# Performance work log

Hardware: AMD Instinct MI355X
Metric: run time of the kernel (lower is better)

## Reference

```python
import jax, jax.numpy as jnp
import numpy as np

NUM_BINS = 15
THRESHOLD = 0.01


def setup_inputs() -> dict:
    key = jax.random.key(0)
    k1, k2 = jax.random.split(key)
    N, C = 500000, 100
    probas = jax.random.uniform(k1, (N, C), dtype=jnp.float32)
    labels = jax.random.randint(k2, (N,), 0, C, dtype=jnp.int64)
    return {"probas": probas, "labels": labels}


def reference(probas, labels):
    # probas: [N, C] float, labels: [N] int
    N, C = probas.shape
    B = NUM_BINS
    bins = jnp.linspace(0.0, 1.0, B + 1, dtype=probas.dtype)  # [B+1]

    # bin index: bins[lo] <= p < bins[lo+1] (side='right' => right edge strict)
    lo = jnp.searchsorted(bins, probas, side='right') - 1      # [N, C]
    lo_c = jnp.clip(lo, 0, B - 1)
    left_edge = bins[lo_c]
    # original uses strict inequalities on BOTH edges, plus threshold filter
    valid = (probas > THRESHOLD) & (lo >= 0) & (lo < B) & (probas > left_edge)
    w = valid.astype(probas.dtype)                              # [N, C]

    # segment id = class * B + bin, flattened over [N, C]
    cols = jnp.broadcast_to(jnp.arange(C), (N, C))
    seg = (cols * B + lo_c).ravel()
    num_seg = C * B

    correct = (labels[:, None] == jnp.arange(C)[None, :]).astype(probas.dtype)

    count = jax.ops.segment_sum(w.ravel(), seg, num_segments=num_seg)
    sum_p = jax.ops.segment_sum((probas * w).ravel(), seg, num_segments=num_seg)
    sum_a = jax.ops.segment_sum((correct * w).ravel(), seg, num_segments=num_seg)

    nan = jnp.asarray(jnp.nan, probas.dtype)
    denom = jnp.maximum(count, 1.0)
    confs = jnp.where(count > 0, sum_p / denom, nan).reshape(C, B)
    accs = jnp.where(count > 0, sum_a / denom, nan).reshape(C, B)
    n_samples = count.reshape(C, B)
    return confs, accs, n_samples
```

## Files before the change

kernel.cpp:

```cpp
#include <hip/hip_runtime.h>

#define NBINS 15
#define NCLS  100
#define NSEG  (NBINS * NCLS)
#define NGRP  64
#define MAXBLK 2048
#define BLK   256
#define SUMSCALE 2048.0f
#define INV15 (1.0f / 15.0f)

typedef float nf4 __attribute__((ext_vector_type(4)));

__device__ __forceinline__ void proc_f4(nf4 v, int i,
                                        const int* __restrict__ labels,
                                        unsigned int* s_pk, unsigned int* s_ac)
{
    int row  = i / 25;
    int col0 = (i - row * 25) * 4;
    int lbl  = labels[row];
    float pv[4] = {v.x, v.y, v.z, v.w};
    #pragma unroll
    for (int j = 0; j < 4; ++j) {
        float p = pv[j];
        int c = col0 + j;
        int k = (int)(p * 15.0f);
        if (k < NBINS && (float)(k + 1) * INV15 <= p)      ++k;
        else if (k > 0 && (float)k * INV15 > p)            --k;
        float left = (float)k * INV15;
        if (p > 0.01f && k < NBINS && p > left) {
            int seg = c * NBINS + k;
            unsigned int pk = (1u << 20) | (unsigned int)(p * SUMSCALE + 0.5f);
            atomicAdd(&s_pk[seg], pk);
            if (lbl == c) atomicAdd(&s_ac[seg], 1u);
        }
    }
}

__global__ __launch_bounds__(BLK) void calib_accum(
    const float* __restrict__ probas,
    const int*   __restrict__ labels,
    unsigned int* __restrict__ partU,
    int total4)
{
    __shared__ unsigned int s_pk[NSEG];
    __shared__ unsigned int s_ac[NSEG];
    const int t = threadIdx.x;
    for (int i = t; i < NSEG; i += BLK) { s_pk[i] = 0u; s_ac[i] = 0u; }
    __syncthreads();

    const nf4* __restrict__ p4 = (const nf4*)probas;
    const int stride = gridDim.x * BLK;
    const int half4  = total4 >> 1;

    for (int i = blockIdx.x * BLK + t; i < half4; i += stride) {
        nf4 a = __builtin_nontemporal_load(&p4[i]);
        nf4 b = __builtin_nontemporal_load(&p4[i + half4]);
        proc_f4(a, i,         labels, s_pk, s_ac);
        proc_f4(b, i + half4, labels, s_pk, s_ac);
    }
    if ((total4 & 1) && blockIdx.x == 0 && t == 0) {
        proc_f4(p4[total4 - 1], total4 - 1, labels, s_pk, s_ac);
    }
    __syncthreads();

    unsigned int* dst = partU + (size_t)blockIdx.x * (2 * NSEG);
    for (int s = t; s < NSEG; s += BLK) {
        dst[s]        = s_pk[s];
        dst[NSEG + s] = s_ac[s];
    }
}

__global__ __launch_bounds__(256) void calib_mid(
    const unsigned int* __restrict__ partU, int nblk, int chunk,
    unsigned int*       __restrict__ partB)
{
    int t = blockIdx.x * 256 + threadIdx.x;
    if (t >= NGRP * NSEG) return;
    int g = t / NSEG;
    int s = t - g * NSEG;
    int b0 = g * chunk;
    int b1 = b0 + chunk; if (b1 > nblk) b1 = nblk;
    unsigned int cnt = 0u, sumq = 0u, acc = 0u;
    for (int b = b0; b < b1; ++b) {
        const unsigned int* src = partU + (size_t)b * (2 * NSEG);
        unsigned int pk = src[s];
        cnt  += pk >> 20;
        sumq += pk & 0xFFFFFu;
        acc  += src[NSEG + s];
    }
    unsigned int* dst = partB + (size_t)g * (3 * NSEG);
    dst[s]            = cnt;
    dst[NSEG + s]     = sumq;
    dst[2 * NSEG + s] = acc;
}

__global__ __launch_bounds__(256) void calib_fin(
    const unsigned int* __restrict__ partB,
    float*              __restrict__ out)
{
    int s = blockIdx.x * 256 + threadIdx.x;
    if (s >= NSEG) return;
    unsigned int cnt = 0u, sumq = 0u, acc = 0u;
    #pragma unroll
    for (int g = 0; g < NGRP; ++g) {
        const unsigned int* src = partB + g * (3 * NSEG);
        cnt  += src[s];
        sumq += src[NSEG + s];
        acc  += src[2 * NSEG + s];
    }
    float conf, accv;
    if (cnt > 0u) {
        float inv = 1.0f / (float)cnt;
        conf = (float)sumq * (1.0f / SUMSCALE) * inv;
        accv = (float)acc * inv;
    } else {
        conf = __int_as_float(0x7fc00000);
        accv = conf;
    }
    out[s]            = conf;
    out[NSEG + s]     = accv;
    out[2 * NSEG + s] = (float)cnt;
}

extern "C" void kernel_launch(void* const* d_in, const int* in_sizes, int n_in,
                              void* d_out, int out_size, void* d_ws, size_t ws_size,
                              hipStream_t stream) {
    const float* probas = (const float*)d_in[0];
    const int*   labels = (const int*)d_in[1];
    float* out = (float*)d_out;
    unsigned int* ws = (unsigned int*)d_ws;

    int total  = in_sizes[0];
    int total4 = total / 4;

    size_t ws_u32 = ws_size / sizeof(unsigned int);
    long long avail = (long long)ws_u32 - (long long)NGRP * 3 * NSEG;
    int nblk = (int)(avail / (2 * NSEG));
    if (nblk > MAXBLK) nblk = MAXBLK;
    if (nblk < 1) nblk = 1;

    unsigned int* partU = ws;
    unsigned int* partB = ws + (size_t)nblk * (2 * NSEG);

    calib_accum<<<nblk, BLK, 0, stream>>>(probas, labels, partU, total4);
    int chunk = (nblk + NGRP - 1) / NGRP;
    calib_mid<<<(NGRP * NSEG + 255) / 256, 256, 0, stream>>>(partU, nblk, chunk, partB);
    calib_fin<<<(NSEG + 255) / 256, 256, 0, stream>>>(partB, out);
}
```

Before: 285.1 us.

## Replace two-stage partial reduction with global atomics from each block

Each accumulation block now adds its shared-memory histogram straight into a single global segment array with atomics, instead of writing per-block partials that a middle kernel reduced. A small zeroing kernel clears the global array first, and the final kernel reads only one copy. This removes the partial-buffer traffic and the middle reduction launch. In exchange there is contention on 4500 global counters from 2048 blocks, and the block count no longer depends on workspace size.

```diff
diff --git a/kernel.cpp b/kernel.cpp
--- a/kernel.cpp
+++ b/kernel.cpp
@@ -3,8 +3,7 @@
 #define NBINS 15
 #define NCLS  100
 #define NSEG  (NBINS * NCLS)
-#define NGRP  64
-#define MAXBLK 2048
+#define NBLK  2048
 #define BLK   256
 #define SUMSCALE 2048.0f
 #define INV15 (1.0f / 15.0f)
@@ -36,10 +35,16 @@
     }
 }
 
+__global__ __launch_bounds__(256) void calib_zero(unsigned int* __restrict__ g)
+{
+    int i = blockIdx.x * 256 + threadIdx.x;
+    if (i < 3 * NSEG) g[i] = 0u;
+}
+
 __global__ __launch_bounds__(BLK) void calib_accum(
     const float* __restrict__ probas,
     const int*   __restrict__ labels,
-    unsigned int* __restrict__ partU,
+    unsigned int* __restrict__ gseg,
     int total4)
 {
     __shared__ unsigned int s_pk[NSEG];
@@ -63,51 +68,26 @@
     }
     __syncthreads();
 
-    unsigned int* dst = partU + (size_t)blockIdx.x * (2 * NSEG);
     for (int s = t; s < NSEG; s += BLK) {
-        dst[s]        = s_pk[s];
-        dst[NSEG + s] = s_ac[s];
+        unsigned int pk = s_pk[s];
+        unsigned int ac = s_ac[s];
+        if (pk) {
+            atomicAdd(&gseg[s],        pk >> 20);
+            atomicAdd(&gseg[NSEG + s], pk & 0xFFFFFu);
+        }
+        if (ac) atomicAdd(&gseg[2 * NSEG + s], ac);
     }
 }
 
-__global__ __launch_bounds__(256) void calib_mid(
-    const unsigned int* __restrict__ partU, int nblk, int chunk,
-    unsigned int*       __restrict__ partB)
-{
-    int t = blockIdx.x * 256 + threadIdx.x;
-    if (t >= NGRP * NSEG) return;
-    int g = t / NSEG;
-    int s = t - g * NSEG;
-    int b0 = g * chunk;
-    int b1 = b0 + chunk; if (b1 > nblk) b1 = nblk;
-    unsigned int cnt = 0u, sumq = 0u, acc = 0u;
-    for (int b = b0; b < b1; ++b) {
-        const unsigned int* src = partU + (size_t)b * (2 * NSEG);
-        unsigned int pk = src[s];
-        cnt  += pk >> 20;
-        sumq += pk & 0xFFFFFu;
-        acc  += src[NSEG + s];
-    }
-    unsigned int* dst = partB + (size_t)g * (3 * NSEG);
-    dst[s]            = cnt;
-    dst[NSEG + s]     = sumq;
-    dst[2 * NSEG + s] = acc;
-}
-
 __global__ __launch_bounds__(256) void calib_fin(
-    const unsigned int* __restrict__ partB,
+    const unsigned int* __restrict__ gseg,
     float*              __restrict__ out)
 {
     int s = blockIdx.x * 256 + threadIdx.x;
     if (s >= NSEG) return;
-    unsigned int cnt = 0u, sumq = 0u, acc = 0u;
-    #pragma unroll
-    for (int g = 0; g < NGRP; ++g) {
-        const unsigned int* src = partB + g * (3 * NSEG);
-        cnt  += src[s];
-        sumq += src[NSEG + s];
-        acc  += src[2 * NSEG + s];
-    }
+    unsigned int cnt  = gseg[s];
+    unsigned int sumq = gseg[NSEG + s];
+    unsigned int acc  = gseg[2 * NSEG + s];
     float conf, accv;
     if (cnt > 0u) {
         float inv = 1.0f / (float)cnt;
@@ -128,22 +108,12 @@
     const float* probas = (const float*)d_in[0];
     const int*   labels = (const int*)d_in[1];
     float* out = (float*)d_out;
-    unsigned int* ws = (unsigned int*)d_ws;
+    unsigned int* gseg = (unsigned int*)d_ws;
 
     int total  = in_sizes[0];
     int total4 = total / 4;
 
-    size_t ws_u32 = ws_size / sizeof(unsigned int);
-    long long avail = (long long)ws_u32 - (long long)NGRP * 3 * NSEG;
-    int nblk = (int)(avail / (2 * NSEG));
-    if (nblk > MAXBLK) nblk = MAXBLK;
-    if (nblk < 1) nblk = 1;
-
-    unsigned int* partU = ws;
-    unsigned int* partB = ws + (size_t)nblk * (2 * NSEG);
-
-    calib_accum<<<nblk, BLK, 0, stream>>>(probas, labels, partU, total4);
-    int chunk = (nblk + NGRP - 1) / NGRP;
-    calib_mid<<<(NGRP * NSEG + 255) / 256, 256, 0, stream>>>(partU, nblk, chunk, partB);
-    calib_fin<<<(NSEG + 255) / 256, 256, 0, stream>>>(partB, out);
+    calib_zero <<<(3 * NSEG + 255) / 256, 256, 0, stream>>>(gseg);
+    calib_accum<<<NBLK, BLK, 0, stream>>>(probas, labels, gseg, total4);
+    calib_fin  <<<(NSEG + 255) / 256, 256, 0, stream>>>(gseg, out);
 }
```

Result: slower. 316.0 us (+10.8%).
